# Performance work log

Hardware: AMD Instinct MI355X
Metric: run time of the kernel (lower is better)

Reference implementation:

```python
import jax, jax.numpy as jnp
import numpy as np

N = 30000   # nodes
E = 600000  # edges (avg degree 20)
H = 128     # hidden_channels
L = 4       # num_layers
G = 64      # graphs in batch


def _init(key, shape, fan_in):
    return (jax.random.normal(key, shape, jnp.float32) / np.sqrt(fan_in)).astype(jnp.float32)


def setup_inputs() -> dict:
    key = jax.random.key(0)
    ks = jax.random.split(key, 24)
    x = jax.random.normal(ks[0], (N, 1), jnp.float32)
    pos = jax.random.normal(ks[1], (N, 3), jnp.float32)
    edge_index = jax.random.randint(ks[2], (2, E), 0, N, dtype=jnp.int32).astype(jnp.int64)
    batch = jnp.sort(jax.random.randint(ks[3], (N,), 0, G, dtype=jnp.int32)).astype(jnp.int64)

    emb_w = _init(ks[4], (1, H), 1)
    emb_b = jnp.zeros((H,), jnp.float32)

    # stacked per-layer params: msg MLP (2H+1 -> H -> H), node MLP (2H -> H -> H)
    msg_w1 = _init(ks[5], (L, 2 * H + 1, H), 2 * H + 1)
    msg_b1 = jnp.zeros((L, H), jnp.float32)
    msg_w2 = _init(ks[6], (L, H, H), H)
    msg_b2 = jnp.zeros((L, H), jnp.float32)
    node_w1 = _init(ks[7], (L, 2 * H, H), 2 * H)
    node_b1 = jnp.zeros((L, H), jnp.float32)
    node_w2 = _init(ks[8], (L, H, H), H)
    node_b2 = jnp.zeros((L, H), jnp.float32)

    out_w1 = _init(ks[9], (H, 32), H)
    out_b1 = jnp.zeros((32,), jnp.float32)
    out_w2 = _init(ks[10], (32, 1), 32)
    out_b2 = jnp.zeros((1,), jnp.float32)

    return {
        "x": x, "pos": pos, "edge_index": edge_index, "batch": batch,
        "emb_w": emb_w, "emb_b": emb_b,
        "msg_w1": msg_w1, "msg_b1": msg_b1, "msg_w2": msg_w2, "msg_b2": msg_b2,
        "node_w1": node_w1, "node_b1": node_b1, "node_w2": node_w2, "node_b2": node_b2,
        "out_w1": out_w1, "out_b1": out_b1, "out_w2": out_w2, "out_b2": out_b2,
    }


def reference(x, pos, edge_index, batch,
              emb_w, emb_b,
              msg_w1, msg_b1, msg_w2, msg_b2,
              node_w1, node_b1, node_w2, node_b2,
              out_w1, out_b1, out_w2, out_b2):
    row, col = edge_index[0], edge_index[1]  # row = source j, col = target i
    # edge scalar: squared distance (computed once, reused across layers)
    dist_sq = jnp.sum((pos[row] - pos[col]) ** 2, axis=-1, keepdims=True)  # [E,1]

    h = x @ emb_w + emb_b  # [N,H]
    for l in range(L):
        x_j = h[row]   # source features
        x_i = h[col]   # target features
        m = jnp.concatenate([x_i, x_j, dist_sq], axis=-1)           # [E, 2H+1]
        m = jax.nn.silu(m @ msg_w1[l] + msg_b1[l]) @ msg_w2[l] + msg_b2[l]  # [E,H]
        aggr = jax.ops.segment_sum(m, col, num_segments=N)          # scatter-add to targets
        nh = jnp.concatenate([h, aggr], axis=-1)                    # [N, 2H]
        h = jax.nn.silu(nh @ node_w1[l] + node_b1[l]) @ node_w2[l] + node_b2[l]
        # dropout omitted for deterministic reference (eval mode)

    g = jax.ops.segment_sum(h, batch, num_segments=G)               # global_add_pool [G,H]
    return jax.nn.silu(g @ out_w1 + out_b1) @ out_w2 + out_b2       # [G,1]
```

## Files before the change

kernel.cpp:

```cpp
#include <hip/hip_runtime.h>

typedef unsigned short u16;
typedef __bf16 bf16x8 __attribute__((ext_vector_type(8)));
typedef float f32x4 __attribute__((ext_vector_type(4)));

#define HN 128
#define TM 64
#define ASTRIDE 136
#define ECH 128

__device__ __forceinline__ u16 f2bf(float f) {
  union { float f; unsigned u; } v; v.f = f;
  unsigned r = v.u + 0x7fffu + ((v.u >> 16) & 1u);
  return (u16)(r >> 16);
}
__device__ __forceinline__ float bf2f(u16 v) {
  union { unsigned u; float f; } x; x.u = ((unsigned)v) << 16; return x.f;
}
__device__ __forceinline__ float bflo(unsigned v) {
  union { unsigned u; float f; } x; x.u = v << 16; return x.f;
}
__device__ __forceinline__ float bfhi(unsigned v) {
  union { unsigned u; float f; } x; x.u = v & 0xffff0000u; return x.f;
}
__device__ __forceinline__ float silu_f(float x) {
  float e = __builtin_amdgcn_exp2f(-1.442695041f * x);
  return x * __builtin_amdgcn_rcpf(1.f + e);
}

__global__ void pack_weights(const float* __restrict__ msg_w1, const float* __restrict__ msg_w2,
                             const float* __restrict__ node_w1, const float* __restrict__ node_w2,
                             u16* __restrict__ pw) {
  int id = blockIdx.x * 256 + threadIdx.x;
  if (id >= 4 * 6 * 16384) return;
  int l = id / (6 * 16384);
  int rem = id % (6 * 16384);
  int m = rem / 16384;
  int e = rem % 16384;
  int kg = e >> 10;
  int n = (e >> 3) & 127;
  int j = e & 7;
  int k = kg * 8 + j;
  float v = 0.f;
  switch (m) {
    case 0: v = msg_w1[(l * 257 + k) * 128 + n]; break;
    case 1: v = msg_w1[(l * 257 + 128 + k) * 128 + n]; break;
    case 2: v = msg_w2[(l * 128 + k) * 128 + n]; break;
    case 3: v = node_w1[(l * 256 + k) * 128 + n]; break;
    case 4: v = node_w1[(l * 256 + 128 + k) * 128 + n]; break;
    case 5: v = node_w2[(l * 128 + k) * 128 + n]; break;
  }
  pw[id] = f2bf(v);
}

__global__ void hist_kernel(const int* __restrict__ eidx, int* __restrict__ deg, int E_) {
  int e = blockIdx.x * 256 + threadIdx.x;
  if (e < E_) atomicAdd(&deg[eidx[E_ + e]], 1);
}

__global__ void scan1_kernel(const int* __restrict__ deg, int* __restrict__ off,
                             int* __restrict__ bsum, int n) {
  __shared__ int s[256];
  int t = threadIdx.x;
  int i = blockIdx.x * 256 + t;
  int v = (i < n) ? deg[i] : 0;
  s[t] = v;
  for (int d = 1; d < 256; d <<= 1) {
    __syncthreads();
    int x = (t >= d) ? s[t - d] : 0;
    __syncthreads();
    s[t] += x;
  }
  __syncthreads();
  if (i < n) off[i] = s[t] - v;
  if (t == 255) bsum[blockIdx.x] = s[255];
}

__global__ void scan2_kernel(int* __restrict__ bsum, int nb) {
  __shared__ int s[256];
  int t = threadIdx.x;
  int v = (t < nb) ? bsum[t] : 0;
  s[t] = v;
  for (int d = 1; d < 256; d <<= 1) {
    __syncthreads();
    int x = (t >= d) ? s[t - d] : 0;
    __syncthreads();
    s[t] += x;
  }
  __syncthreads();
  if (t < nb) bsum[t] = s[t] - v;
}

__global__ void scan3_kernel(int* __restrict__ off, const int* __restrict__ bsum,
                             int* __restrict__ cursor, int n) {
  int i = blockIdx.x * 256 + threadIdx.x;
  if (i < n) {
    int v = off[i] + bsum[blockIdx.x];
    off[i] = v;
    cursor[i] = v;
  }
}

__global__ void scatter_kernel(const int* __restrict__ eidx, const float* __restrict__ pos,
                               int* __restrict__ cursor, int* __restrict__ es, int E_) {
  int e = blockIdx.x * 256 + threadIdx.x;
  if (e >= E_) return;
  int sr = eidx[e], tg = eidx[E_ + e];
  float dx = pos[sr * 3 + 0] - pos[tg * 3 + 0];
  float dy = pos[sr * 3 + 1] - pos[tg * 3 + 1];
  float dz = pos[sr * 3 + 2] - pos[tg * 3 + 2];
  float d = dx * dx + dy * dy + dz * dz;
  int p = atomicAdd(&cursor[tg], 1);
  es[3 * p + 0] = sr;
  es[3 * p + 1] = tg;
  ((float*)es)[3 * p + 2] = d;
}

__device__ __forceinline__ void gemm64(const u16* s_A, const u16* s_W,
                                       int w, int quad, int m16, f32x4 acc[8]) {
#pragma unroll
  for (int ks = 0; ks < 4; ks++) {
    bf16x8 a = *(const bf16x8*)&s_A[(w * 16 + m16) * ASTRIDE + ks * 32 + quad * 8];
#pragma unroll
    for (int ct = 0; ct < 8; ct++) {
      bf16x8 b = *(const bf16x8*)&s_W[(ks * 4 + quad) * 1024 + (ct * 16 + m16) * 8];
      acc[ct] = __builtin_amdgcn_mfma_f32_16x16x32_bf16(a, b, acc[ct], 0, 0, 0);
    }
  }
}

__global__ __launch_bounds__(256) void proj_kernel(
    const float* __restrict__ x, const float* __restrict__ emb_w,
    const float* __restrict__ emb_b, u16* __restrict__ hbf,
    u16* __restrict__ Pout, u16* __restrict__ Qout,
    const u16* __restrict__ pw, const float* __restrict__ b1, int nnodes) {
  __shared__ __align__(16) u16 s_A[TM * ASTRIDE];
  __shared__ __align__(16) u16 s_W[16384];
  const int t = threadIdx.x;
  const int w = t >> 6, lane = t & 63, quad = lane >> 4, m16 = lane & 15;
  const int tile0 = blockIdx.x * TM;
  {
    int r = t >> 2, qo = (t & 3) * 32;
    int node = tile0 + r;
    if (node >= nnodes) node = nnodes - 1;
    float xv = x[node];
    u16 hv[32];
#pragma unroll
    for (int i = 0; i < 32; i++) hv[i] = f2bf(xv * emb_w[qo + i] + emb_b[qo + i]);
    u16* dst = s_A + r * ASTRIDE + qo;
#pragma unroll
    for (int i = 0; i < 4; i++) *(int4*)(dst + i * 8) = *(int4*)(hv + i * 8);
    u16* gd = hbf + (size_t)node * HN + qo;
#pragma unroll
    for (int i = 0; i < 4; i++) *(int4*)(gd + i * 8) = *(int4*)(hv + i * 8);
  }
  {
    const int4* src = (const int4*)pw;
    int4* dst = (int4*)s_W;
#pragma unroll
    for (int i = 0; i < 8; i++) dst[t + i * 256] = src[t + i * 256];
  }
  __syncthreads();
  f32x4 acc[8];
#pragma unroll
  for (int ct = 0; ct < 8; ct++) acc[ct] = {0.f, 0.f, 0.f, 0.f};
  gemm64(s_A, s_W, w, quad, m16, acc);
  __syncthreads();
  {
    const int4* src = (const int4*)(pw + 16384);
    int4* dst = (int4*)s_W;
#pragma unroll
    for (int i = 0; i < 8; i++) dst[t + i * 256] = src[t + i * 256];
  }
  float bb[8];
#pragma unroll
  for (int ct = 0; ct < 8; ct++) bb[ct] = b1[ct * 16 + m16];
#pragma unroll
  for (int ct = 0; ct < 8; ct++)
#pragma unroll
    for (int j = 0; j < 4; j++) {
      int n = tile0 + w * 16 + quad * 4 + j;
      if (n < nnodes) Pout[n * HN + ct * 16 + m16] = f2bf(acc[ct][j] + bb[ct]);
    }
  __syncthreads();
#pragma unroll
  for (int ct = 0; ct < 8; ct++) acc[ct] = {0.f, 0.f, 0.f, 0.f};
  gemm64(s_A, s_W, w, quad, m16, acc);
#pragma unroll
  for (int ct = 0; ct < 8; ct++)
#pragma unroll
    for (int j = 0; j < 4; j++) {
      int n = tile0 + w * 16 + quad * 4 + j;
      if (n < nnodes) Qout[n * HN + ct * 16 + m16] = f2bf(acc[ct][j]);
    }
}

__device__ __forceinline__ void edge_step(
    int tg, float dd, unsigned qv,
    int& cur, float& p0, float& p1, float& s0, float& s1,
    const u16* __restrict__ P, float* __restrict__ S, int cp,
    float wd0, float wd1, int tprev, int tnext) {
  if (tg != cur) {
    if (cur >= 0) {
      float* dst = &S[(size_t)cur * HN + cp];
      if (cur == tprev || cur == tnext) {
        atomicAdd(dst, s0);
        atomicAdd(dst + 1, s1);
      } else {
        float2 v = {s0, s1};
        *(float2*)dst = v;
      }
    }
    cur = tg; s0 = 0.f; s1 = 0.f;
    int cg = tg < 0 ? 0 : tg;
    unsigned pv = *(const unsigned*)&P[(size_t)cg * HN + cp];
    p0 = bflo(pv); p1 = bfhi(pv);
  }
  float x0 = p0 + bflo(qv) + dd * wd0;
  float x1 = p1 + bfhi(qv) + dd * wd1;
  s0 += silu_f(x0);
  s1 += silu_f(x1);
}

__global__ __launch_bounds__(256) void edge_kernel(
    const u16* __restrict__ P, const u16* __restrict__ Q,
    float* __restrict__ S, const float* __restrict__ w1d,
    const int* __restrict__ es, int E_) {
  __shared__ int s_src[ECH + 4];
  __shared__ int s_tgt[ECH + 4];
  __shared__ float s_dist[ECH + 4];

  const int t = threadIdx.x;
  const int e0 = blockIdx.x * ECH;
  if (t < ECH) {
    int e = e0 + t;
    if (e < E_) {
      s_src[t] = es[3 * e + 0];
      s_tgt[t] = es[3 * e + 1];
      s_dist[t] = ((const float*)es)[3 * e + 2];
    } else {
      s_src[t] = 0; s_tgt[t] = -1; s_dist[t] = 0.f;
    }
  } else if (t < ECH + 4) {
    s_src[t] = 0; s_tgt[t] = -1; s_dist[t] = 0.f;
  }
  __syncthreads();

  const int lane = t & 63;
  const int w = t >> 6;
  const int cp = lane * 2;
  const int a = w * 32;
  const float2 wdv = *(const float2*)&w1d[cp];
  const float wd0 = wdv.x, wd1 = wdv.y;

  int tprev, tnext;
  if (w == 0) tprev = (e0 > 0) ? es[3 * (e0 - 1) + 1] : -2;
  else tprev = s_tgt[a - 1];
  if (w == 3) tnext = (e0 + ECH < E_) ? es[3 * (e0 + ECH) + 1] : -2;
  else tnext = s_tgt[a + 32];

  int t0 = s_tgt[a + 0], t1 = s_tgt[a + 1], t2 = s_tgt[a + 2], t3 = s_tgt[a + 3];
  float d0 = s_dist[a + 0], d1 = s_dist[a + 1], d2 = s_dist[a + 2], d3 = s_dist[a + 3];
  unsigned q0 = *(const unsigned*)&Q[(size_t)s_src[a + 0] * HN + cp];
  unsigned q1 = *(const unsigned*)&Q[(size_t)s_src[a + 1] * HN + cp];
  unsigned q2 = *(const unsigned*)&Q[(size_t)s_src[a + 2] * HN + cp];
  unsigned q3 = *(const unsigned*)&Q[(size_t)s_src[a + 3] * HN + cp];

  int cur = -1;
  float s0 = 0.f, s1 = 0.f, p0 = 0.f, p1 = 0.f;

#pragma unroll
  for (int i = a; i < a + 32; i += 4) {
    int n0 = s_tgt[i + 4], n1 = s_tgt[i + 5], n2 = s_tgt[i + 6], n3 = s_tgt[i + 7];
    float f0 = s_dist[i + 4], f1 = s_dist[i + 5], f2 = s_dist[i + 6], f3 = s_dist[i + 7];
    unsigned m0 = *(const unsigned*)&Q[(size_t)s_src[i + 4] * HN + cp];
    unsigned m1 = *(const unsigned*)&Q[(size_t)s_src[i + 5] * HN + cp];
    unsigned m2 = *(const unsigned*)&Q[(size_t)s_src[i + 6] * HN + cp];
    unsigned m3 = *(const unsigned*)&Q[(size_t)s_src[i + 7] * HN + cp];

    edge_step(t0, d0, q0, cur, p0, p1, s0, s1, P, S, cp, wd0, wd1, tprev, tnext);
    edge_step(t1, d1, q1, cur, p0, p1, s0, s1, P, S, cp, wd0, wd1, tprev, tnext);
    edge_step(t2, d2, q2, cur, p0, p1, s0, s1, P, S, cp, wd0, wd1, tprev, tnext);
    edge_step(t3, d3, q3, cur, p0, p1, s0, s1, P, S, cp, wd0, wd1, tprev, tnext);

    t0 = n0; t1 = n1; t2 = n2; t3 = n3;
    d0 = f0; d1 = f1; d2 = f2; d3 = f3;
    q0 = m0; q1 = m1; q2 = m2; q3 = m3;
  }

  if (cur >= 0) {
    float* dst = &S[(size_t)cur * HN + cp];
    if (cur == tprev || cur == tnext) {
      atomicAdd(dst, s0);
      atomicAdd(dst + 1, s1);
    } else {
      float2 v = {s0, s1};
      *(float2*)dst = v;
    }
  }
}

template <bool FUSE>
__global__ __launch_bounds__(256) void node_kernel(
    const u16* __restrict__ hbf, float* __restrict__ S, const int* __restrict__ deg,
    u16* __restrict__ hout, const u16* __restrict__ pw2m, const float* __restrict__ b2m,
    const u16* __restrict__ pwn, const float* __restrict__ b1, const float* __restrict__ b2,
    const u16* __restrict__ pw_next, const float* __restrict__ b1_next,
    u16* __restrict__ Pout, u16* __restrict__ Qout, int nnodes) {
  __shared__ __align__(16) u16 s_A[TM * ASTRIDE];
  __shared__ __align__(16) u16 s_W[16384];
  const int t = threadIdx.x;
  const int w = t >> 6, lane = t & 63, quad = lane >> 4, m16 = lane & 15;
  const int tile0 = blockIdx.x * TM;
  const int r_ = t >> 2, qo_ = (t & 3) * 32;
  int node_ = tile0 + r_;
  if (node_ >= nnodes) node_ = nnodes - 1;

  {
    const int4* src = (const int4*)pw2m;
    int4* dst = (int4*)s_W;
#pragma unroll
    for (int i = 0; i < 8; i++) dst[t + i * 256] = src[t + i * 256];
  }
  {
    const float4* src = (const float4*)(S + (size_t)node_ * HN + qo_);
    u16* dst = s_A + r_ * ASTRIDE + qo_;
#pragma unroll
    for (int i = 0; i < 8; i++) {
      float4 v = src[i];
      ushort4 o;
      o.x = f2bf(v.x); o.y = f2bf(v.y); o.z = f2bf(v.z); o.w = f2bf(v.w);
      *(ushort4*)(dst + i * 4) = o;
    }
  }
  __syncthreads();
  {
    float4 z = {0.f, 0.f, 0.f, 0.f};
    float4* zd = (float4*)(S + (size_t)node_ * HN + qo_);
#pragma unroll
    for (int i = 0; i < 8; i++) zd[i] = z;
  }

  f32x4 acc[8];
#pragma unroll
  for (int ct = 0; ct < 8; ct++) acc[ct] = {0.f, 0.f, 0.f, 0.f};
  gemm64(s_A, s_W, w, quad, m16, acc);

  {
    float b2r[8];
#pragma unroll
    for (int ct = 0; ct < 8; ct++) b2r[ct] = b2m[ct * 16 + m16];
    float degv[4];
#pragma unroll
    for (int j = 0; j < 4; j++) {
      int n = tile0 + w * 16 + quad * 4 + j;
      if (n >= nnodes) n = nnodes - 1;
      degv[j] = (float)deg[n];
    }
#pragma unroll
    for (int ct = 0; ct < 8; ct++)
#pragma unroll
      for (int j = 0; j < 4; j++) {
        int row = w * 16 + quad * 4 + j;
        s_A[row * ASTRIDE + ct * 16 + m16] = f2bf(acc[ct][j] + degv[j] * b2r[ct]);
      }
  }
  __syncthreads();
  {
    const int4* src = (const int4*)(pwn + 16384);
    int4* dst = (int4*)s_W;
#pragma unroll
    for (int i = 0; i < 8; i++) dst[t + i * 256] = src[t + i * 256];
  }
  __syncthreads();

#pragma unroll
  for (int ct = 0; ct < 8; ct++) acc[ct] = {0.f, 0.f, 0.f, 0.f};
  gemm64(s_A, s_W, w, quad, m16, acc);
  __syncthreads();

  {
    const int4* src = (const int4*)pwn;
    int4* dst = (int4*)s_W;
#pragma unroll
    for (int i = 0; i < 8; i++) dst[t + i * 256] = src[t + i * 256];
  }
  {
    const int4* src = (const int4*)(hbf + (size_t)node_ * HN + qo_);
    int4* dst = (int4*)(s_A + r_ * ASTRIDE + qo_);
#pragma unroll
    for (int i = 0; i < 4; i++) dst[i] = src[i];
  }
  __syncthreads();
  gemm64(s_A, s_W, w, quad, m16, acc);
  __syncthreads();

  {
    const int4* src = (const int4*)(pwn + 32768);
    int4* dst = (int4*)s_W;
#pragma unroll
    for (int i = 0; i < 8; i++) dst[t + i * 256] = src[t + i * 256];
  }
  {
    float bb1[8];
#pragma unroll
    for (int ct = 0; ct < 8; ct++) bb1[ct] = b1[ct * 16 + m16];
#pragma unroll
    for (int ct = 0; ct < 8; ct++)
#pragma unroll
      for (int j = 0; j < 4; j++) {
        int row = w * 16 + quad * 4 + j;
        float xv = acc[ct][j] + bb1[ct];
        s_A[row * ASTRIDE + ct * 16 + m16] = f2bf(silu_f(xv));
      }
  }
  __syncthreads();

#pragma unroll
  for (int ct = 0; ct < 8; ct++) acc[ct] = {0.f, 0.f, 0.f, 0.f};
  gemm64(s_A, s_W, w, quad, m16, acc);

  float bb2[8];
#pragma unroll
  for (int ct = 0; ct < 8; ct++) bb2[ct] = b2[ct * 16 + m16];
#pragma unroll
  for (int ct = 0; ct < 8; ct++)
#pragma unroll
    for (int j = 0; j < 4; j++) {
      int row = w * 16 + quad * 4 + j;
      int n = tile0 + row;
      if (n < nnodes) hout[n * HN + ct * 16 + m16] = f2bf(acc[ct][j] + bb2[ct]);
    }

  if (FUSE) {
#pragma unroll
    for (int ct = 0; ct < 8; ct++)
#pragma unroll
      for (int j = 0; j < 4; j++) {
        int row = w * 16 + quad * 4 + j;
        s_A[row * ASTRIDE + ct * 16 + m16] = f2bf(acc[ct][j] + bb2[ct]);
      }
    __syncthreads();
    {
      const int4* src = (const int4*)pw_next;
      int4* dst = (int4*)s_W;
#pragma unroll
      for (int i = 0; i < 8; i++) dst[t + i * 256] = src[t + i * 256];
    }
    __syncthreads();
#pragma unroll
    for (int ct = 0; ct < 8; ct++) acc[ct] = {0.f, 0.f, 0.f, 0.f};
    gemm64(s_A, s_W, w, quad, m16, acc);
    {
      float bbn[8];
#pragma unroll
      for (int ct = 0; ct < 8; ct++) bbn[ct] = b1_next[ct * 16 + m16];
#pragma unroll
      for (int ct = 0; ct < 8; ct++)
#pragma unroll
        for (int j = 0; j < 4; j++) {
          int n = tile0 + w * 16 + quad * 4 + j;
          if (n < nnodes) Pout[n * HN + ct * 16 + m16] = f2bf(acc[ct][j] + bbn[ct]);
        }
    }
    __syncthreads();
    {
      const int4* src = (const int4*)(pw_next + 16384);
      int4* dst = (int4*)s_W;
#pragma unroll
      for (int i = 0; i < 8; i++) dst[t + i * 256] = src[t + i * 256];
    }
    __syncthreads();
#pragma unroll
    for (int ct = 0; ct < 8; ct++) acc[ct] = {0.f, 0.f, 0.f, 0.f};
    gemm64(s_A, s_W, w, quad, m16, acc);
#pragma unroll
    for (int ct = 0; ct < 8; ct++)
#pragma unroll
      for (int j = 0; j < 4; j++) {
        int n = tile0 + w * 16 + quad * 4 + j;
        if (n < nnodes) Qout[n * HN + ct * 16 + m16] = f2bf(acc[ct][j]);
      }
  }
}

__global__ __launch_bounds__(256) void pool_kernel(
    const u16* __restrict__ h, const int* __restrict__ batch,
    float* __restrict__ g, int N) {
  __shared__ int s_b[64];
  const int t = threadIdx.x;
  const int n0 = blockIdx.x * 64;
  if (t < 64) {
    int n = n0 + t;
    s_b[t] = (n < N) ? batch[n] : -1;
  }
  __syncthreads();
  const int cp = (t & 63) * 2;
  const int rg = t >> 6;
  int cur = -1;
  float s0 = 0.f, s1 = 0.f;
#pragma unroll 4
  for (int i = 0; i < 16; i++) {
    int r = rg * 16 + i;
    int b = s_b[r];
    if (b < 0) break;
    if (b != cur) {
      if (cur >= 0) {
        atomicAdd(&g[cur * HN + cp], s0);
        atomicAdd(&g[cur * HN + cp + 1], s1);
      }
      cur = b; s0 = 0.f; s1 = 0.f;
    }
    unsigned v = *(const unsigned*)&h[(size_t)(n0 + r) * HN + cp];
    s0 += bf2f((u16)(v & 0xffffu));
    s1 += bf2f((u16)(v >> 16));
  }
  if (cur >= 0) {
    atomicAdd(&g[cur * HN + cp], s0);
    atomicAdd(&g[cur * HN + cp + 1], s1);
  }
}

__global__ __launch_bounds__(64) void out_kernel(
    const float* __restrict__ g, const float* __restrict__ w1,
    const float* __restrict__ b1, const float* __restrict__ w2,
    const float* __restrict__ b2, float* __restrict__ out) {
  const int gi = blockIdx.x;
  const int t = threadIdx.x;
  const int c = t & 31, kh = t >> 5;
  float s = 0.f;
  for (int k = kh * 64; k < kh * 64 + 64; k++)
    s += g[gi * HN + k] * w1[k * 32 + c];
  s += __shfl_down(s, 32);
  float r = 0.f;
  if (kh == 0) r = silu_f(s + b1[c]) * w2[c];
  r += __shfl_down(r, 16);
  r += __shfl_down(r, 8);
  r += __shfl_down(r, 4);
  r += __shfl_down(r, 2);
  r += __shfl_down(r, 1);
  if (t == 0) out[gi] = r + b2[0];
}

extern "C" void kernel_launch(void* const* d_in, const int* in_sizes, int n_in,
                              void* d_out, int out_size, void* d_ws, size_t ws_size,
                              hipStream_t stream) {
  const float* x = (const float*)d_in[0];
  const float* pos = (const float*)d_in[1];
  const int* eidx = (const int*)d_in[2];
  const int* batch = (const int*)d_in[3];
  const float* emb_w = (const float*)d_in[4];
  const float* emb_b = (const float*)d_in[5];
  const float* msg_w1 = (const float*)d_in[6];
  const float* msg_b1 = (const float*)d_in[7];
  const float* msg_w2 = (const float*)d_in[8];
  const float* msg_b2 = (const float*)d_in[9];
  const float* node_w1 = (const float*)d_in[10];
  const float* node_b1 = (const float*)d_in[11];
  const float* node_w2 = (const float*)d_in[12];
  const float* node_b2 = (const float*)d_in[13];
  const float* out_w1 = (const float*)d_in[14];
  const float* out_b1 = (const float*)d_in[15];
  const float* out_w2 = (const float*)d_in[16];
  const float* out_b2 = (const float*)d_in[17];
  float* outp = (float*)d_out;

  const int N = 30000, E = 600000, G = 64;
  const size_t NH = (size_t)N * HN;

  u16* hA = (u16*)d_ws;
  u16* hB = hA + NH;
  u16* Pp = hB + NH;
  u16* Qp = Pp + NH;
  float* S = (float*)(Qp + NH);
  int* es = (int*)(S + NH);
  int* deg = es + 3 * (size_t)E;
  int* off = deg + N;
  int* cursor = off + N;
  int* bsum = cursor + N;
  float* g = (float*)(bsum + 128);
  u16* pw = (u16*)(g + G * HN);

  const int NB = (N + 255) / 256;
  const int NTB = (N + TM - 1) / TM;

  pack_weights<<<(4 * 6 * 16384 + 255) / 256, 256, 0, stream>>>(msg_w1, msg_w2, node_w1, node_w2, pw);

  hipMemsetAsync(deg, 0, N * sizeof(int), stream);
  hist_kernel<<<(E + 255) / 256, 256, 0, stream>>>(eidx, deg, E);
  scan1_kernel<<<NB, 256, 0, stream>>>(deg, off, bsum, N);
  scan2_kernel<<<1, 256, 0, stream>>>(bsum, NB);
  scan3_kernel<<<NB, 256, 0, stream>>>(off, bsum, cursor, N);
  scatter_kernel<<<(E + 255) / 256, 256, 0, stream>>>(eidx, pos, cursor, es, E);

  hipMemsetAsync(S, 0, NH * sizeof(float), stream);

  proj_kernel<<<NTB, 256, 0, stream>>>(x, emb_w, emb_b, hA, Pp, Qp, pw, msg_b1, N);

  u16* hcur = hA;
  u16* hnext = hB;
  for (int l = 0; l < 4; l++) {
    const u16* pwl = pw + (size_t)(l * 6) * 16384;
    edge_kernel<<<(E + ECH - 1) / ECH, 256, 0, stream>>>(
        Pp, Qp, S,
        msg_w1 + (size_t)(l * 257 + 256) * 128,
        es, E);
    if (l < 3) {
      const u16* pw_next = pw + (size_t)((l + 1) * 6) * 16384;
      node_kernel<true><<<NTB, 256, 0, stream>>>(
          hcur, S, deg, hnext, pwl + 2 * 16384, msg_b2 + l * 128,
          pwl + 3 * 16384, node_b1 + l * 128, node_b2 + l * 128,
          pw_next, msg_b1 + (l + 1) * 128, Pp, Qp, N);
    } else {
      node_kernel<false><<<NTB, 256, 0, stream>>>(
          hcur, S, deg, hnext, pwl + 2 * 16384, msg_b2 + l * 128,
          pwl + 3 * 16384, node_b1 + l * 128, node_b2 + l * 128,
          nullptr, nullptr, nullptr, nullptr, N);
    }
    u16* tmp = hcur; hcur = hnext; hnext = tmp;
  }

  hipMemsetAsync(g, 0, (size_t)G * HN * sizeof(float), stream);
  pool_kernel<<<(N + 63) / 64, 256, 0, stream>>>(hcur, batch, g, N);
  out_kernel<<<G, 64, 0, stream>>>(g, out_w1, out_b1, out_w2, out_b2, outp);
}
```

Measured before the change: 450.8 us.

## Fold msg_w2 into node_w1 aggregate half and enlarge edge chunk

```diff
diff --git a/kernel.cpp b/kernel.cpp
--- a/kernel.cpp
+++ b/kernel.cpp
@@ -7,7 +7,7 @@
 #define HN 128
 #define TM 64
 #define ASTRIDE 136
-#define ECH 128
+#define ECH 256
 
 __device__ __forceinline__ u16 f2bf(float f) {
   union { float f; unsigned u; } v; v.f = f;
@@ -53,6 +53,69 @@
   pw[id] = f2bf(v);
 }
 
+__device__ __forceinline__ void gemm64(const u16* s_A, const u16* s_W,
+                                       int w, int quad, int m16, f32x4 acc[8]) {
+#pragma unroll
+  for (int ks = 0; ks < 4; ks++) {
+    bf16x8 a = *(const bf16x8*)&s_A[(w * 16 + m16) * ASTRIDE + ks * 32 + quad * 8];
+#pragma unroll
+    for (int ct = 0; ct < 8; ct++) {
+      bf16x8 b = *(const bf16x8*)&s_W[(ks * 4 + quad) * 1024 + (ct * 16 + m16) * 8];
+      acc[ct] = __builtin_amdgcn_mfma_f32_16x16x32_bf16(a, b, acc[ct], 0, 0, 0);
+    }
+  }
+}
+
+__global__ __launch_bounds__(256) void fold_kernel(
+    const float* __restrict__ msg_w2, const float* __restrict__ node_w1,
+    const float* __restrict__ msg_b2, const u16* __restrict__ pw,
+    u16* __restrict__ pwc, float* __restrict__ vc) {
+  __shared__ __align__(16) u16 s_A[TM * ASTRIDE];
+  __shared__ __align__(16) u16 s_W[16384];
+  const int t = threadIdx.x;
+  const int w = t >> 6, lane = t & 63, quad = lane >> 4, m16 = lane & 15;
+  const int b = blockIdx.x, l = b >> 1, half = b & 1;
+  const int tile0 = half * 64;
+
+  {
+    int r = t >> 2, qo = (t & 3) * 32;
+    const float4* src = (const float4*)(msg_w2 + (size_t)(l * 128 + tile0 + r) * 128 + qo);
+    u16* dst = s_A + r * ASTRIDE + qo;
+#pragma unroll
+    for (int i = 0; i < 8; i++) {
+      float4 v = src[i];
+      ushort4 o;
+      o.x = f2bf(v.x); o.y = f2bf(v.y); o.z = f2bf(v.z); o.w = f2bf(v.w);
+      *(ushort4*)(dst + i * 4) = o;
+    }
+  }
+  {
+    const int4* src = (const int4*)(pw + (size_t)(l * 6 + 4) * 16384);
+    int4* dst = (int4*)s_W;
+#pragma unroll
+    for (int i = 0; i < 8; i++) dst[t + i * 256] = src[t + i * 256];
+  }
+  __syncthreads();
+  f32x4 acc[8];
+#pragma unroll
+  for (int ct = 0; ct < 8; ct++) acc[ct] = {0.f, 0.f, 0.f, 0.f};
+  gemm64(s_A, s_W, w, quad, m16, acc);
+#pragma unroll
+  for (int ct = 0; ct < 8; ct++)
+#pragma unroll
+    for (int j = 0; j < 4; j++) {
+      int k = tile0 + w * 16 + quad * 4 + j;
+      int n = ct * 16 + m16;
+      pwc[(size_t)l * 16384 + (k >> 3) * 1024 + n * 8 + (k & 7)] = f2bf(acc[ct][j]);
+    }
+  if (half == 0 && t < 128) {
+    float s = 0.f;
+    for (int np = 0; np < 128; np++)
+      s += msg_b2[l * 128 + np] * node_w1[(size_t)(l * 256 + 128 + np) * 128 + t];
+    vc[l * 128 + t] = s;
+  }
+}
+
 __global__ void hist_kernel(const int* __restrict__ eidx, int* __restrict__ deg, int E_) {
   int e = blockIdx.x * 256 + threadIdx.x;
   if (e < E_) atomicAdd(&deg[eidx[E_ + e]], 1);
@@ -114,19 +177,6 @@
   es[3 * p + 0] = sr;
   es[3 * p + 1] = tg;
   ((float*)es)[3 * p + 2] = d;
-}
-
-__device__ __forceinline__ void gemm64(const u16* s_A, const u16* s_W,
-                                       int w, int quad, int m16, f32x4 acc[8]) {
-#pragma unroll
-  for (int ks = 0; ks < 4; ks++) {
-    bf16x8 a = *(const bf16x8*)&s_A[(w * 16 + m16) * ASTRIDE + ks * 32 + quad * 8];
-#pragma unroll
-    for (int ct = 0; ct < 8; ct++) {
-      bf16x8 b = *(const bf16x8*)&s_W[(ks * 4 + quad) * 1024 + (ct * 16 + m16) * 8];
-      acc[ct] = __builtin_amdgcn_mfma_f32_16x16x32_bf16(a, b, acc[ct], 0, 0, 0);
-    }
-  }
 }
 
 __global__ __launch_bounds__(256) void proj_kernel(
@@ -232,7 +282,7 @@
 
   const int t = threadIdx.x;
   const int e0 = blockIdx.x * ECH;
-  if (t < ECH) {
+  {
     int e = e0 + t;
     if (e < E_) {
       s_src[t] = es[3 * e + 0];
@@ -241,15 +291,14 @@
     } else {
       s_src[t] = 0; s_tgt[t] = -1; s_dist[t] = 0.f;
     }
-  } else if (t < ECH + 4) {
-    s_src[t] = 0; s_tgt[t] = -1; s_dist[t] = 0.f;
+    if (t < 4) { s_src[ECH + t] = 0; s_tgt[ECH + t] = -1; s_dist[ECH + t] = 0.f; }
   }
   __syncthreads();
 
   const int lane = t & 63;
   const int w = t >> 6;
   const int cp = lane * 2;
-  const int a = w * 32;
+  const int a = w * 64;
   const float2 wdv = *(const float2*)&w1d[cp];
   const float wd0 = wdv.x, wd1 = wdv.y;
 
@@ -257,7 +306,7 @@
   if (w == 0) tprev = (e0 > 0) ? es[3 * (e0 - 1) + 1] : -2;
   else tprev = s_tgt[a - 1];
   if (w == 3) tnext = (e0 + ECH < E_) ? es[3 * (e0 + ECH) + 1] : -2;
-  else tnext = s_tgt[a + 32];
+  else tnext = s_tgt[a + 64];
 
   int t0 = s_tgt[a + 0], t1 = s_tgt[a + 1], t2 = s_tgt[a + 2], t3 = s_tgt[a + 3];
   float d0 = s_dist[a + 0], d1 = s_dist[a + 1], d2 = s_dist[a + 2], d3 = s_dist[a + 3];
@@ -269,8 +318,8 @@
   int cur = -1;
   float s0 = 0.f, s1 = 0.f, p0 = 0.f, p1 = 0.f;
 
-#pragma unroll
-  for (int i = a; i < a + 32; i += 4) {
+#pragma unroll 4
+  for (int i = a; i < a + 64; i += 4) {
     int n0 = s_tgt[i + 4], n1 = s_tgt[i + 5], n2 = s_tgt[i + 6], n3 = s_tgt[i + 7];
     float f0 = s_dist[i + 4], f1 = s_dist[i + 5], f2 = s_dist[i + 6], f3 = s_dist[i + 7];
     unsigned m0 = *(const unsigned*)&Q[(size_t)s_src[i + 4] * HN + cp];
@@ -303,7 +352,7 @@
 template <bool FUSE>
 __global__ __launch_bounds__(256) void node_kernel(
     const u16* __restrict__ hbf, float* __restrict__ S, const int* __restrict__ deg,
-    u16* __restrict__ hout, const u16* __restrict__ pw2m, const float* __restrict__ b2m,
+    u16* __restrict__ hout, const u16* __restrict__ pwc, const float* __restrict__ vc,
     const u16* __restrict__ pwn, const float* __restrict__ b1, const float* __restrict__ b2,
     const u16* __restrict__ pw_next, const float* __restrict__ b1_next,
     u16* __restrict__ Pout, u16* __restrict__ Qout, int nnodes) {
@@ -317,7 +366,7 @@
   if (node_ >= nnodes) node_ = nnodes - 1;
 
   {
-    const int4* src = (const int4*)pw2m;
+    const int4* src = (const int4*)pwc;
     int4* dst = (int4*)s_W;
 #pragma unroll
     for (int i = 0; i < 8; i++) dst[t + i * 256] = src[t + i * 256];
@@ -332,24 +381,48 @@
       o.x = f2bf(v.x); o.y = f2bf(v.y); o.z = f2bf(v.z); o.w = f2bf(v.w);
       *(ushort4*)(dst + i * 4) = o;
     }
-  }
-  __syncthreads();
-  {
     float4 z = {0.f, 0.f, 0.f, 0.f};
     float4* zd = (float4*)(S + (size_t)node_ * HN + qo_);
 #pragma unroll
     for (int i = 0; i < 8; i++) zd[i] = z;
   }
+  __syncthreads();
 
   f32x4 acc[8];
 #pragma unroll
   for (int ct = 0; ct < 8; ct++) acc[ct] = {0.f, 0.f, 0.f, 0.f};
   gemm64(s_A, s_W, w, quad, m16, acc);
-
-  {
-    float b2r[8];
-#pragma unroll
-    for (int ct = 0; ct < 8; ct++) b2r[ct] = b2m[ct * 16 + m16];
+  __syncthreads();
+
+  {
+    const int4* src = (const int4*)pwn;
+    int4* dst = (int4*)s_W;
+#pragma unroll
+    for (int i = 0; i < 8; i++) dst[t + i * 256] = src[t + i * 256];
+  }
+  {
+    const int4* src = (const int4*)(hbf + (size_t)node_ * HN + qo_);
+    int4* dst = (int4*)(s_A + r_ * ASTRIDE + qo_);
+#pragma unroll
+    for (int i = 0; i < 4; i++) dst[i] = src[i];
+  }
+  __syncthreads();
+  gemm64(s_A, s_W, w, quad, m16, acc);
+  __syncthreads();
+
+  {
+    const int4* src = (const int4*)(pwn + 32768);
+    int4* dst = (int4*)s_W;
+#pragma unroll
+    for (int i = 0; i < 8; i++) dst[t + i * 256] = src[t + i * 256];
+  }
+  {
+    float bb1[8], vcr[8];
+#pragma unroll
+    for (int ct = 0; ct < 8; ct++) {
+      bb1[ct] = b1[ct * 16 + m16];
+      vcr[ct] = vc[ct * 16 + m16];
+    }
     float degv[4];
 #pragma unroll
     for (int j = 0; j < 4; j++) {
@@ -362,55 +435,7 @@
 #pragma unroll
       for (int j = 0; j < 4; j++) {
         int row = w * 16 + quad * 4 + j;
-        s_A[row * ASTRIDE + ct * 16 + m16] = f2bf(acc[ct][j] + degv[j] * b2r[ct]);
-      }
-  }
-  __syncthreads();
-  {
-    const int4* src = (const int4*)(pwn + 16384);
-    int4* dst = (int4*)s_W;
-#pragma unroll
-    for (int i = 0; i < 8; i++) dst[t + i * 256] = src[t + i * 256];
-  }
-  __syncthreads();
-
-#pragma unroll
-  for (int ct = 0; ct < 8; ct++) acc[ct] = {0.f, 0.f, 0.f, 0.f};
-  gemm64(s_A, s_W, w, quad, m16, acc);
-  __syncthreads();
-
-  {
-    const int4* src = (const int4*)pwn;
-    int4* dst = (int4*)s_W;
-#pragma unroll
-    for (int i = 0; i < 8; i++) dst[t + i * 256] = src[t + i * 256];
-  }
-  {
-    const int4* src = (const int4*)(hbf + (size_t)node_ * HN + qo_);
-    int4* dst = (int4*)(s_A + r_ * ASTRIDE + qo_);
-#pragma unroll
-    for (int i = 0; i < 4; i++) dst[i] = src[i];
-  }
-  __syncthreads();
-  gemm64(s_A, s_W, w, quad, m16, acc);
-  __syncthreads();
-
-  {
-    const int4* src = (const int4*)(pwn + 32768);
-    int4* dst = (int4*)s_W;
-#pragma unroll
-    for (int i = 0; i < 8; i++) dst[t + i * 256] = src[t + i * 256];
-  }
-  {
-    float bb1[8];
-#pragma unroll
-    for (int ct = 0; ct < 8; ct++) bb1[ct] = b1[ct * 16 + m16];
-#pragma unroll
-    for (int ct = 0; ct < 8; ct++)
-#pragma unroll
-      for (int j = 0; j < 4; j++) {
-        int row = w * 16 + quad * 4 + j;
-        float xv = acc[ct][j] + bb1[ct];
+        float xv = acc[ct][j] + bb1[ct] + degv[j] * vcr[ct];
         s_A[row * ASTRIDE + ct * 16 + m16] = f2bf(silu_f(xv));
       }
   }
@@ -580,11 +605,14 @@
   int* bsum = cursor + N;
   float* g = (float*)(bsum + 128);
   u16* pw = (u16*)(g + G * HN);
+  u16* pwc = pw + (size_t)4 * 6 * 16384;
+  float* vcb = (float*)(pwc + (size_t)4 * 16384);
 
   const int NB = (N + 255) / 256;
   const int NTB = (N + TM - 1) / TM;
 
   pack_weights<<<(4 * 6 * 16384 + 255) / 256, 256, 0, stream>>>(msg_w1, msg_w2, node_w1, node_w2, pw);
+  fold_kernel<<<8, 256, 0, stream>>>(msg_w2, node_w1, msg_b2, pw, pwc, vcb);
 
   hipMemsetAsync(deg, 0, N * sizeof(int), stream);
   hist_kernel<<<(E + 255) / 256, 256, 0, stream>>>(eidx, deg, E);
@@ -608,12 +636,12 @@
     if (l < 3) {
       const u16* pw_next = pw + (size_t)((l + 1) * 6) * 16384;
       node_kernel<true><<<NTB, 256, 0, stream>>>(
-          hcur, S, deg, hnext, pwl + 2 * 16384, msg_b2 + l * 128,
+          hcur, S, deg, hnext, pwc + (size_t)l * 16384, vcb + l * 128,
           pwl + 3 * 16384, node_b1 + l * 128, node_b2 + l * 128,
           pw_next, msg_b1 + (l + 1) * 128, Pp, Qp, N);
     } else {
       node_kernel<false><<<NTB, 256, 0, stream>>>(
-          hcur, S, deg, hnext, pwl + 2 * 16384, msg_b2 + l * 128,
+          hcur, S, deg, hnext, pwc + (size_t)l * 16384, vcb + l * 128,
           pwl + 3 * 16384, node_b1 + l * 128, node_b2 + l * 128,
           nullptr, nullptr, nullptr, nullptr, N);
     }
```

Measured after the change: 428.6 us. -4.9%, faster.
